# Optimization experiments

Measured on AMD Instinct MI355X. Metric: run time of the kernel, lower is better.

The kernel has to match this reference:

```python
import jax, jax.numpy as jnp
import numpy as np

N_QUBITS = 11
DIM = 2 ** N_QUBITS
GAIN = 2 ** 0.5
LRMUL = 1.0
W_MUL = GAIN * 5 ** (-0.5) * LRMUL  # use_wscale=True path


def _build_unitary(weight):
    """Overall circuit unitary. Per qubit q the circuit applies rx, ry, rz
    (left_to_right composition => Rz @ Ry @ Rx on that qubit's subspace).
    Gates on distinct qubits commute, so the sequential product of expanded
    gates equals the kron over qubits of the per-qubit composite 2x2 gate,
    with qubit 0 as the leftmost kron factor (matches gate_expand_1toN)."""
    w = (weight * W_MUL).reshape(N_QUBITS, 3)
    half = w / 2
    c = jnp.cos(half)
    s = jnp.sin(half)
    cx, sx = c[:, 0], s[:, 0]
    cy, sy = c[:, 1], s[:, 1]
    ez = jnp.exp(-1j * half[:, 2])  # e^{-i phi_z / 2}
    zeros = jnp.zeros_like(ez)
    # [n, 2, 2] gate stacks (complex64)
    rx = jnp.stack([jnp.stack([cx + 0j, -1j * sx], -1),
                    jnp.stack([-1j * sx, cx + 0j], -1)], -2)
    ry = jnp.stack([jnp.stack([cy + 0j, -sy + 0j], -1),
                    jnp.stack([sy + 0j, cy + 0j], -1)], -2)
    rz = jnp.stack([jnp.stack([ez, zeros], -1),
                    jnp.stack([zeros, jnp.conj(ez)], -1)], -2)
    g = rz @ ry @ rx  # [n, 2, 2] composite per-qubit gate
    U = g[0]
    for q in range(1, N_QUBITS):  # loop over fixed small n_qubits is fine
        U = jnp.kron(U, g[q])
    return U  # [DIM, DIM] complex64


def setup_inputs() -> dict:
    key = jax.random.key(0)
    kx, kw = jax.random.split(key)
    x = jax.random.normal(kx, (DIM, DIM), dtype=jnp.float32)
    weight = jax.random.uniform(kw, (N_QUBITS * 3,), dtype=jnp.float32,
                                minval=0.0, maxval=2.0 * np.pi)
    return {"x": x, "weight": weight}


def reference(x, weight):
    U = _build_unitary(weight)
    xc = x.astype(jnp.complex64)
    # queryQ_out = U @ x @ U^dagger
    return U @ xc @ jnp.conj(U).T
```

## Files before the change

### kernel.cpp

```cpp
#include <hip/hip_runtime.h>
#include <hip/hip_fp16.h>


#define DIM 2048
#define NQ 11

typedef float v2f __attribute__((ext_vector_type(2)));

__device__ __forceinline__ int swz(int j) { return j ^ ((j >> 5) & 31); }

__device__ __forceinline__ float2 cmul(float2 a, float2 b) {
    return make_float2(a.x * b.x - a.y * b.y, a.x * b.y + a.y * b.x);
}

__device__ __forceinline__ v2f pkmul_swap(v2f s, v2f g) {
    v2f d;
    asm("v_pk_mul_f32 %0, %1, %2 op_sel:[1,0] op_sel_hi:[0,1]"
        : "=v"(d) : "v"(s), "v"(g));
    return d;
}
__device__ __forceinline__ v2f pkfma(v2f s0, v2f s1, v2f c) {
    v2f d;
    asm("v_pk_fma_f32 %0, %1, %2, %3" : "=v"(d) : "v"(s0), "v"(s1), "v"(c));
    return d;
}
__device__ __forceinline__ v2f pkfma_swap(v2f s0, v2f s1, v2f c) {
    v2f d;
    asm("v_pk_fma_f32 %0, %1, %2, %3 op_sel:[1,0,0] op_sel_hi:[0,1,1]"
        : "=v"(d) : "v"(s0), "v"(s1), "v"(c));
    return d;
}

struct PkGate {
    v2f x00, y00, x01, y01, x10, y10, x11, y11;
};

__device__ __forceinline__ void make_gate(const float* __restrict__ w, int q,
                                          int conj, float2* out4) {
    const float WM = 0.632455532033675866f;
    float hx = 0.5f * WM * w[q * 3 + 0];
    float hy = 0.5f * WM * w[q * 3 + 1];
    float hz = 0.5f * WM * w[q * 3 + 2];
    float cx, sx, cy, sy, cz, sz;
    sincosf(hx, &sx, &cx);
    sincosf(hy, &sy, &cy);
    sincosf(hz, &sz, &cz);
    float2 m00 = make_float2(cy * cx,  sy * sx);
    float2 m01 = make_float2(-sy * cx, -cy * sx);
    float2 m10 = make_float2(sy * cx,  -cy * sx);
    float2 m11 = make_float2(cy * cx,  -sy * sx);
    float2 ez  = make_float2(cz, -sz);
    float2 ezc = make_float2(cz,  sz);
    float2 g00 = cmul(ez, m00);
    float2 g01 = cmul(ez, m01);
    float2 g10 = cmul(ezc, m10);
    float2 g11 = cmul(ezc, m11);
    float sgn = conj ? -1.f : 1.f;
    out4[0] = make_float2(g00.x, sgn * g00.y);
    out4[1] = make_float2(g01.x, sgn * g01.y);
    out4[2] = make_float2(g10.x, sgn * g10.y);
    out4[3] = make_float2(g11.x, sgn * g11.y);
}

__device__ __forceinline__ void build_pk_gates(const float* __restrict__ wt,
                                               int t, int conj,
                                               v2f (*gsh)[8]) {
    if (t < NQ) {
        float2 e[4];
        make_gate(wt, t, conj, e);
#pragma unroll
        for (int k = 0; k < 4; ++k) {
            v2f px = {e[k].x, e[k].x};
            v2f py = {-e[k].y, e[k].y};
            gsh[t][2 * k + 0] = px;
            gsh[t][2 * k + 1] = py;
        }
    }
}

__device__ __forceinline__ void load_pkgate(const v2f (*gsh)[8], int q,
                                            PkGate& G) {
    G.x00 = gsh[q][0]; G.y00 = gsh[q][1];
    G.x01 = gsh[q][2]; G.y01 = gsh[q][3];
    G.x10 = gsh[q][4]; G.y10 = gsh[q][5];
    G.x11 = gsh[q][6]; G.y11 = gsh[q][7];
}

__device__ __forceinline__ void bfly(float2& A, float2& B, const PkGate& G) {
    v2f a = __builtin_bit_cast(v2f, A), b = __builtin_bit_cast(v2f, B);
    v2f t;
    t = pkmul_swap(b, G.y01);
    t = pkfma(b, G.x01, t);
    t = pkfma_swap(a, G.y00, t);
    A = __builtin_bit_cast(float2, pkfma(a, G.x00, t));
    t = pkmul_swap(b, G.y11);
    t = pkfma(b, G.x11, t);
    t = pkfma_swap(a, G.y10, t);
    B = __builtin_bit_cast(float2, pkfma(a, G.x10, t));
}

template <int ST>
__device__ __forceinline__ void stage16(float2* v, const PkGate& G) {
#pragma unroll
    for (int m = 0; m < 16; ++m)
        if (!(m & ST)) bfly(v[m], v[m + ST], G);
}

__device__ __forceinline__ unsigned pack_h2(float2 v) {
    __half2 h = __float22half2_rn(v);
    return *reinterpret_cast<unsigned*>(&h);
}
__device__ __forceinline__ float2 unpack_h2(unsigned u) {
    __half2 h = *reinterpret_cast<__half2*>(&u);
    return __half22float2(h);
}

__global__ __launch_bounds__(256, 2) void rowpassK1(
    const float* __restrict__ X, unsigned* __restrict__ Y,
    const float* __restrict__ wt) {
    __shared__ float pRe[2 * DIM];
    __shared__ float pIm[2 * DIM];
    __shared__ v2f gsh[NQ][8];
    int t = threadIdx.x;
    build_pk_gates(wt, t, 1, gsh);
    __syncthreads();

    int u = t & 127, rv = t >> 7;
    int base = rv * DIM;
    int row = blockIdx.x * 2 + rv;
    const float* xrow = X + (size_t)row * DIM;

    float xr[16];
#pragma unroll
    for (int m = 0; m < 16; ++m) xr[m] = xrow[u + (m << 7)];

    float e00x = gsh[3][0][0], e00y = gsh[3][1][1];
    float e01x = gsh[3][2][0], e01y = gsh[3][3][1];
    float e10x = gsh[3][4][0], e10y = gsh[3][5][1];
    float e11x = gsh[3][6][0], e11y = gsh[3][7][1];
    float2 v[16];
#pragma unroll
    for (int m = 0; m < 16; m += 2) {
        float a = xr[m], b = xr[m + 1];
        v[m]     = make_float2(e00x * a + e01x * b, e00y * a + e01y * b);
        v[m + 1] = make_float2(e10x * a + e11x * b, e10y * a + e11y * b);
    }
    PkGate G;
    load_pkgate(gsh, 2, G); stage16<2>(v, G);
    load_pkgate(gsh, 1, G); stage16<4>(v, G);
    load_pkgate(gsh, 0, G); stage16<8>(v, G);

#pragma unroll
    for (int m = 0; m < 16; ++m) {
        int a = base + swz(u + (m << 7));
        pRe[a] = v[m].x; pIm[a] = v[m].y;
    }
    __syncthreads();

    int uLo = u & 7, uHi = u >> 3;
#pragma unroll
    for (int m = 0; m < 16; ++m) {
        int a = base + swz(uLo + (m << 3) + (uHi << 7));
        v[m] = make_float2(pRe[a], pIm[a]);
    }
    load_pkgate(gsh, 7, G); stage16<1>(v, G);
    load_pkgate(gsh, 6, G); stage16<2>(v, G);
    load_pkgate(gsh, 5, G); stage16<4>(v, G);
    load_pkgate(gsh, 4, G); stage16<8>(v, G);
#pragma unroll
    for (int m = 0; m < 16; ++m) {
        int a = base + swz(uLo + (m << 3) + (uHi << 7));
        pRe[a] = v[m].x; pIm[a] = v[m].y;
    }
    __syncthreads();

#pragma unroll
    for (int m = 0; m < 16; ++m) {
        int a = base + swz(m + (u << 4));
        v[m] = make_float2(pRe[a], pIm[a]);
    }
    load_pkgate(gsh, 10, G); stage16<1>(v, G);
    load_pkgate(gsh, 9, G);  stage16<2>(v, G);
    load_pkgate(gsh, 8, G);  stage16<4>(v, G);

    unsigned* yp = Y + (size_t)(2 * u) * (DIM * 8) + (size_t)row * 8;
    uint4 pk0, pk1;
    pk0.x = pack_h2(v[0]); pk0.y = pack_h2(v[1]);
    pk0.z = pack_h2(v[2]); pk0.w = pack_h2(v[3]);
    pk1.x = pack_h2(v[4]); pk1.y = pack_h2(v[5]);
    pk1.z = pack_h2(v[6]); pk1.w = pack_h2(v[7]);
    *reinterpret_cast<uint4*>(yp) = pk0;
    *reinterpret_cast<uint4*>(yp + 4) = pk1;
    unsigned* yp2 = yp + DIM * 8;
    pk0.x = pack_h2(v[8]);  pk0.y = pack_h2(v[9]);
    pk0.z = pack_h2(v[10]); pk0.w = pack_h2(v[11]);
    pk1.x = pack_h2(v[12]); pk1.y = pack_h2(v[13]);
    pk1.z = pack_h2(v[14]); pk1.w = pack_h2(v[15]);
    *reinterpret_cast<uint4*>(yp2) = pk0;
    *reinterpret_cast<uint4*>(yp2 + 4) = pk1;
}

__global__ __launch_bounds__(1024, 4) void colfused(
    const unsigned* __restrict__ Y, float* __restrict__ Out,
    const float* __restrict__ wt, int writeComplex) {
    __shared__ float pRe[DIM * 9];
    __shared__ float pIm[DIM * 9];
    __shared__ v2f gsh[NQ][8];
    int t = threadIdx.x;
    build_pk_gates(wt, t, 0, gsh);
    __syncthreads();

    int c = t & 7, u = t >> 3;
    const unsigned* yb = Y + (size_t)blockIdx.x * (DIM * 8);

    float2 v[16];
    PkGate G;
#pragma unroll
    for (int m = 0; m < 16; ++m)
        v[m] = unpack_h2(yb[(u + (m << 7)) * 8 + c]);

    load_pkgate(gsh, 3, G); stage16<1>(v, G);
    load_pkgate(gsh, 2, G); stage16<2>(v, G);
    load_pkgate(gsh, 1, G); stage16<4>(v, G);
    load_pkgate(gsh, 0, G); stage16<8>(v, G);

#pragma unroll
    for (int m = 0; m < 16; ++m) {
        int a = (u + (m << 7)) * 9 + c;
        pRe[a] = v[m].x; pIm[a] = v[m].y;
    }
    __syncthreads();

    int uLo = u & 7, uHi = u >> 3;
#pragma unroll
    for (int m = 0; m < 16; ++m) {
        int a = (uLo + (m << 3) + (uHi << 7)) * 9 + c;
        v[m] = make_float2(pRe[a], pIm[a]);
    }
    load_pkgate(gsh, 7, G); stage16<1>(v, G);
    load_pkgate(gsh, 6, G); stage16<2>(v, G);
    load_pkgate(gsh, 5, G); stage16<4>(v, G);
    load_pkgate(gsh, 4, G); stage16<8>(v, G);
#pragma unroll
    for (int m = 0; m < 16; ++m) {
        int a = (uLo + (m << 3) + (uHi << 7)) * 9 + c;
        pRe[a] = v[m].x; pIm[a] = v[m].y;
    }
    __syncthreads();

#pragma unroll
    for (int m = 0; m < 16; ++m) {
        int a = (m + (u << 4)) * 9 + c;
        v[m] = make_float2(pRe[a], pIm[a]);
    }
    load_pkgate(gsh, 10, G); stage16<1>(v, G);
    load_pkgate(gsh, 9, G);  stage16<2>(v, G);
    load_pkgate(gsh, 8, G);  stage16<4>(v, G);

    int j = blockIdx.x * 8 + c;
    if (!writeComplex) {
#pragma unroll
        for (int m = 0; m < 16; ++m)
            Out[(size_t)(m + (u << 4)) * DIM + j] = v[m].x;
    } else {
        float2* o2 = (float2*)Out;
#pragma unroll
        for (int m = 0; m < 16; ++m)
            o2[(size_t)(m + (u << 4)) * DIM + j] = v[m];
    }
}

extern "C" void kernel_launch(void* const* d_in, const int* in_sizes, int n_in,
                              void* d_out, int out_size, void* d_ws,
                              size_t ws_size, hipStream_t stream) {
    const float* X = (const float*)d_in[0];
    const float* wt = (const float*)d_in[1];
    float* out = (float*)d_out;
    unsigned* Y = (unsigned*)d_ws;

    rowpassK1<<<DIM / 2, 256, 0, stream>>>(X, Y, wt);
    int wc = (out_size >= 2 * DIM * DIM) ? 1 : 0;
    colfused<<<DIM / 8, 1024, 0, stream>>>(Y, out, wt, wc);
}
```

Before: 38.58 us.

## Pack LDS staging to half2 and remap block-to-strip order in colfused

Result: faster. 36.45 us (-5.5%).

```diff
diff --git a/kernel.cpp b/kernel.cpp
--- a/kernel.cpp
+++ b/kernel.cpp
@@ -203,15 +203,16 @@
 __global__ __launch_bounds__(1024, 4) void colfused(
     const unsigned* __restrict__ Y, float* __restrict__ Out,
     const float* __restrict__ wt, int writeComplex) {
-    __shared__ float pRe[DIM * 9];
-    __shared__ float pIm[DIM * 9];
+    __shared__ unsigned pk[DIM * 9];
     __shared__ v2f gsh[NQ][8];
     int t = threadIdx.x;
     build_pk_gates(wt, t, 0, gsh);
     __syncthreads();
 
+    int strip = ((blockIdx.x & 7) << 5) + (blockIdx.x >> 3);
+
     int c = t & 7, u = t >> 3;
-    const unsigned* yb = Y + (size_t)blockIdx.x * (DIM * 8);
+    const unsigned* yb = Y + (size_t)strip * (DIM * 8);
 
     float2 v[16];
     PkGate G;
@@ -225,39 +226,31 @@
     load_pkgate(gsh, 0, G); stage16<8>(v, G);
 
 #pragma unroll
-    for (int m = 0; m < 16; ++m) {
-        int a = (u + (m << 7)) * 9 + c;
-        pRe[a] = v[m].x; pIm[a] = v[m].y;
-    }
+    for (int m = 0; m < 16; ++m)
+        pk[(u + (m << 7)) * 9 + c] = pack_h2(v[m]);
     __syncthreads();
 
     int uLo = u & 7, uHi = u >> 3;
 #pragma unroll
-    for (int m = 0; m < 16; ++m) {
-        int a = (uLo + (m << 3) + (uHi << 7)) * 9 + c;
-        v[m] = make_float2(pRe[a], pIm[a]);
-    }
+    for (int m = 0; m < 16; ++m)
+        v[m] = unpack_h2(pk[(uLo + (m << 3) + (uHi << 7)) * 9 + c]);
     load_pkgate(gsh, 7, G); stage16<1>(v, G);
     load_pkgate(gsh, 6, G); stage16<2>(v, G);
     load_pkgate(gsh, 5, G); stage16<4>(v, G);
     load_pkgate(gsh, 4, G); stage16<8>(v, G);
 #pragma unroll
-    for (int m = 0; m < 16; ++m) {
-        int a = (uLo + (m << 3) + (uHi << 7)) * 9 + c;
-        pRe[a] = v[m].x; pIm[a] = v[m].y;
-    }
-    __syncthreads();
-
-#pragma unroll
-    for (int m = 0; m < 16; ++m) {
-        int a = (m + (u << 4)) * 9 + c;
-        v[m] = make_float2(pRe[a], pIm[a]);
-    }
+    for (int m = 0; m < 16; ++m)
+        pk[(uLo + (m << 3) + (uHi << 7)) * 9 + c] = pack_h2(v[m]);
+    __syncthreads();
+
+#pragma unroll
+    for (int m = 0; m < 16; ++m)
+        v[m] = unpack_h2(pk[(m + (u << 4)) * 9 + c]);
     load_pkgate(gsh, 10, G); stage16<1>(v, G);
     load_pkgate(gsh, 9, G);  stage16<2>(v, G);
     load_pkgate(gsh, 8, G);  stage16<4>(v, G);
 
-    int j = blockIdx.x * 8 + c;
+    int j = strip * 8 + c;
     if (!writeComplex) {
 #pragma unroll
         for (int m = 0; m < 16; ++m)
```
